# Optimization experiments

Measured on AMD Instinct MI355X. Metric: run time of the kernel, lower is better.

## Reference

```python
import jax, jax.numpy as jnp
import numpy as np

WIN = 7           # window height/width
DIM = 192         # channels
HEADS = 6
HEAD_DIM = DIM // HEADS  # 32
B_WIN = 4096      # num_windows * batch
NW = 64           # windows per image (for shift mask)
N = WIN * WIN     # 49 tokens per window
THETA = 10.0


def _init_rope_freqs(key):
    # init_random_2d_freqs: mag = 1/theta^(arange(0,hd,4)[:hd//4]/hd)
    mag = 1.0 / THETA ** (jnp.arange(0, HEAD_DIM, 4)[: HEAD_DIM // 4].astype(jnp.float32) / HEAD_DIM)
    ang = jax.random.uniform(key, (HEADS, 1)) * 2.0 * jnp.pi
    fx = jnp.concatenate([mag * jnp.cos(ang), mag * jnp.cos(jnp.pi / 2 + ang)], axis=-1)  # [H, hd/2]
    fy = jnp.concatenate([mag * jnp.sin(ang), mag * jnp.sin(jnp.pi / 2 + ang)], axis=-1)
    return jnp.stack([fx, fy], axis=0)  # [2, H, hd/2]


def setup_inputs() -> dict:
    key = jax.random.key(0)
    ks = jax.random.split(key, 6)
    x = jax.random.normal(ks[0], (B_WIN, N, DIM), dtype=jnp.float32)
    mask = jnp.zeros((NW, N, N), dtype=jnp.float32)  # 0/-inf shift mask (zeros: no shift)
    qkv_w = jax.random.normal(ks[1], (3 * DIM, DIM), dtype=jnp.float32) * 0.02
    qkv_b = jnp.zeros((3 * DIM,), dtype=jnp.float32)
    proj_w = jax.random.normal(ks[2], (DIM, DIM), dtype=jnp.float32) * 0.02
    proj_b = jnp.zeros((DIM,), dtype=jnp.float32)
    rope_freqs = _init_rope_freqs(ks[3])
    return {"x": x, "mask": mask, "qkv_w": qkv_w, "qkv_b": qkv_b,
            "proj_w": proj_w, "proj_b": proj_b, "rope_freqs": rope_freqs}


def _rope_angles(rope_freqs):
    # t_x = t % end_x, t_y = t // end_x over the flattened window grid
    t = jnp.arange(N, dtype=jnp.float32)
    t_x = jnp.mod(t, WIN)
    t_y = jnp.floor_divide(t, WIN)
    # angle[h, n, d] = t_x[n]*fx[h,d] + t_y[n]*fy[h,d]  -> [H, N, hd/2]
    ang = (t_x[None, :, None] * rope_freqs[0][:, None, :]
           + t_y[None, :, None] * rope_freqs[1][:, None, :])
    return jnp.cos(ang), jnp.sin(ang)


def _apply_rope(u, cos, sin):
    # u: [B, H, N, hd]; complex multiply on (even, odd) pairs
    b, h, n, d = u.shape
    ur = u.reshape(b, h, n, d // 2, 2)
    re = ur[..., 0] * cos - ur[..., 1] * sin
    im = ur[..., 0] * sin + ur[..., 1] * cos
    return jnp.stack([re, im], axis=-1).reshape(b, h, n, d)


def reference(x, mask, qkv_w, qkv_b, proj_w, proj_b, rope_freqs):
    B_, n, C = x.shape
    H, hd = HEADS, HEAD_DIM
    scale = hd ** -0.5
    qkv = (x @ qkv_w.T + qkv_b).reshape(B_, n, 3, H, hd)
    qkv = jnp.transpose(qkv, (2, 0, 3, 1, 4))          # [3, B, H, N, hd]
    q, k, v = qkv[0] * scale, qkv[1], qkv[2]
    cos, sin = _rope_angles(rope_freqs)                 # [H, N, hd/2]
    q = _apply_rope(q, cos, sin)
    k = _apply_rope(k, cos, sin)
    attn = jnp.einsum('bhnd,bhmd->bhnm', q, k)          # [B, H, N, N]
    nW = mask.shape[0]
    attn = attn.reshape(B_ // nW, nW, H, n, n) + mask[None, :, None]
    attn = jax.nn.softmax(attn.reshape(B_, H, n, n), axis=-1)
    out = jnp.einsum('bhnm,bhmd->bhnd', attn, v)        # [B, H, N, hd]
    out = jnp.transpose(out, (0, 2, 1, 3)).reshape(B_, n, C)
    return out @ proj_w.T + proj_b
```

## Files before the change

kernel.cpp:

```cpp
#include <hip/hip_runtime.h>

#define NTOK 49
#define DIM 192
#define HEADS 6
#define NWIN 64
#define NBLK 4096

typedef unsigned short u16;
typedef short bf16x8 __attribute__((ext_vector_type(8)));
typedef unsigned short u16x4 __attribute__((ext_vector_type(4)));
typedef unsigned short u16x8 __attribute__((ext_vector_type(8)));
typedef float f32x4 __attribute__((ext_vector_type(4)));

#define Q_OFF    0
#define K_OFF    20000
#define PS_OFF   40000
#define VT_OFF   49216
#define XS_OFF   49216
#define OS_OFF   20000
#define MK_OFF   76864
#define LDS_TOTAL 81764

#define QKVW_ELEMS (3 * DIM * DIM)
#define PROJW_ELEMS (DIM * DIM)

__device__ __forceinline__ float bf2f(u16 u) {
    union { unsigned int i; float f; } x; x.i = ((unsigned int)u) << 16; return x.f;
}
__device__ __forceinline__ u16 f2bf(float f) {
    union { float f; unsigned int u; } x; x.f = f;
    unsigned int u = x.u;
    u += 0x7fffu + ((u >> 16) & 1u);
    return (u16)(u >> 16);
}

extern "C" __global__ void __launch_bounds__(256)
convert_weights(const float* __restrict__ qkv_w, const float* __restrict__ proj_w,
                u16* __restrict__ ws) {
    int i = (blockIdx.x * 256 + threadIdx.x) * 4;
    if (i >= QKVW_ELEMS + PROJW_ELEMS) return;
    const float* s = (i < QKVW_ELEMS) ? (qkv_w + i) : (proj_w + (i - QKVW_ELEMS));
    float4 v = *(const float4*)s;
    ushort4 o;
    o.x = f2bf(v.x); o.y = f2bf(v.y); o.z = f2bf(v.z); o.w = f2bf(v.w);
    *(ushort4*)(ws + i) = o;
}

extern "C" __global__ void __launch_bounds__(256, 2)
fused_win_attn(const float* __restrict__ x, const float* __restrict__ mask,
               const u16* __restrict__ wsq, const float* __restrict__ qkv_b,
               const u16* __restrict__ wsp, const float* __restrict__ proj_b,
               const float* __restrict__ rfreq, float* __restrict__ out)
{
    extern __shared__ __align__(16) char smem[];
    u16* qsm = (u16*)(smem + Q_OFF);
    u16* ksm = (u16*)(smem + K_OFF);
    u16* ps  = (u16*)(smem + PS_OFF);
    u16* vt  = (u16*)(smem + VT_OFF);
    u16* xs  = (u16*)(smem + XS_OFF);
    float* os = (float*)(smem + OS_OFF);
    u16* ao  = (u16*)(smem + Q_OFF);
    u16* mk  = (u16*)(smem + MK_OFF);

    const int tid  = threadIdx.x;
    const int wave = tid >> 6;
    const int lane = tid & 63;
    const int ln   = lane & 15;
    const int quad = lane >> 4;
    const int blk  = blockIdx.x;
    const int widx = blk & (NWIN - 1);
    const float* xg = x + (long)blk * NTOK * DIM;

    const f32x4 fzero = {0.f, 0.f, 0.f, 0.f};

    for (int i = tid; i < NTOK * 48; i += 256) {
        int r = i / 48, c = (i % 48) * 4;
        float4 v = *(const float4*)(xg + r * DIM + c);
        u16x4 o = { f2bf(v.x), f2bf(v.y), f2bf(v.z), f2bf(v.w) };
        *(u16x4*)(xs + r * 200 + c) = o;
    }
    {
        u16x8 zz = {0,0,0,0,0,0,0,0};
        for (int i = tid; i < 15 * 25; i += 256) {
            int r = 49 + i / 25, c = (i % 25) * 8;
            *(u16x8*)(xs + r * 200 + c) = zz;
        }
        if (tid < 50) {
            int c = (tid % 25) * 8;
            u16* base = (tid < 25) ? qsm : ksm;
            *(u16x8*)(base + 49 * 200 + c) = zz;
        }
    }
    for (int i = tid; i < NTOK * NTOK; i += 256) {
        int n = i / NTOK, m = i % NTOK;
        mk[n * 50 + m] = f2bf(mask[widx * (NTOK * NTOK) + i]);
    }
    __syncthreads();

    bf16x8 bfrag[6][4];
    #pragma unroll
    for (int kk = 0; kk < 6; kk++)
        #pragma unroll
        for (int nt = 0; nt < 4; nt++)
            bfrag[kk][nt] = *(const bf16x8*)(xs + (nt * 16 + ln) * 200 + kk * 32 + quad * 8);
    __syncthreads();

    const float scale = 0.17677669529663687f;
    for (int jt = wave; jt < 36; jt += 4) {
        bf16x8 af[6];
        const u16* wr = wsq + (jt * 16 + ln) * DIM + quad * 8;
        #pragma unroll
        for (int kk = 0; kk < 6; kk++) af[kk] = *(const bf16x8*)(wr + kk * 32);
        f32x4 acc[4];
        #pragma unroll
        for (int nt = 0; nt < 4; nt++) acc[nt] = fzero;
        #pragma unroll
        for (int kk = 0; kk < 6; kk++)
            #pragma unroll
            for (int nt = 0; nt < 4; nt++)
                acc[nt] = __builtin_amdgcn_mfma_f32_16x16x32_bf16(af[kk], bfrag[kk][nt], acc[nt], 0, 0, 0);

        int j0 = jt * 16 + quad * 4;
        int qkvi = j0 / DIM;
        int c0 = j0 % DIM;
        int h  = c0 >> 5;
        int p0 = (c0 & 31) >> 1;
        float b0 = qkv_b[j0],   b1 = qkv_b[j0+1];
        float b2 = qkv_b[j0+2], b3 = qkv_b[j0+3];
        float fx0 = rfreq[h*16+p0],   fy0 = rfreq[96+h*16+p0];
        float fx1 = rfreq[h*16+p0+1], fy1 = rfreq[96+h*16+p0+1];
        #pragma unroll
        for (int nt = 0; nt < 4; nt++) {
            int t = nt * 16 + ln;
            float v0 = acc[nt][0] + b0;
            float v1 = acc[nt][1] + b1;
            float v2 = acc[nt][2] + b2;
            float v3 = acc[nt][3] + b3;
            if (qkvi < 2) {
                float tx = (float)(t % 7), ty = (float)(t / 7);
                float a0 = tx * fx0 + ty * fy0;
                float a1 = tx * fx1 + ty * fy1;
                float s0, c0s, s1, c1s;
                __sincosf(a0, &s0, &c0s);
                __sincosf(a1, &s1, &c1s);
                float r0 = v0 * c0s - v1 * s0;
                float i0 = v0 * s0  + v1 * c0s;
                float r1 = v2 * c1s - v3 * s1;
                float i1 = v2 * s1  + v3 * c1s;
                if (qkvi == 0) { r0 *= scale; i0 *= scale; r1 *= scale; i1 *= scale; }
                if (t < NTOK) {
                    u16x4 pk = { f2bf(r0), f2bf(i0), f2bf(r1), f2bf(i1) };
                    u16* dst = (qkvi == 0 ? qsm : ksm) + t * 200 + c0;
                    *(u16x4*)dst = pk;
                }
            } else {
                float w0 = (t < NTOK) ? v0 : 0.f;
                float w1 = (t < NTOK) ? v1 : 0.f;
                float w2 = (t < NTOK) ? v2 : 0.f;
                float w3 = (t < NTOK) ? v3 : 0.f;
                vt[(c0+0)*72 + t] = f2bf(w0);
                vt[(c0+1)*72 + t] = f2bf(w1);
                vt[(c0+2)*72 + t] = f2bf(w2);
                vt[(c0+3)*72 + t] = f2bf(w3);
            }
        }
    }
    __syncthreads();

    int qrow = wave * 16 + ln; if (qrow > NTOK) qrow = NTOK;
    for (int h = 0; h < HEADS; h++) {
        f32x4 s4[4];
        bf16x8 aq = *(const bf16x8*)(qsm + qrow * 200 + h * 32 + quad * 8);
        #pragma unroll
        for (int nt = 0; nt < 4; nt++) {
            int krow = nt * 16 + ln; if (krow > NTOK) krow = NTOK;
            bf16x8 bk = *(const bf16x8*)(ksm + krow * 200 + h * 32 + quad * 8);
            s4[nt] = __builtin_amdgcn_mfma_f32_16x16x32_bf16(aq, bk, fzero, 0, 0, 0);
        }
        #pragma unroll
        for (int nt = 0; nt < 4; nt++) {
            int m = nt * 16 + ln;
            #pragma unroll
            for (int r = 0; r < 4; r++) {
                int n = wave * 16 + quad * 4 + r;
                if (m >= NTOK) s4[nt][r] = -1e30f;
                else if (n < NTOK) s4[nt][r] += bf2f(mk[n * 50 + m]);
            }
        }
        float mx[4], sm[4], rs[4];
        #pragma unroll
        for (int r = 0; r < 4; r++) {
            float v = fmaxf(fmaxf(s4[0][r], s4[1][r]), fmaxf(s4[2][r], s4[3][r]));
            #pragma unroll
            for (int d = 1; d < 16; d <<= 1) v = fmaxf(v, __shfl_xor(v, d));
            mx[r] = v; sm[r] = 0.f;
        }
        #pragma unroll
        for (int nt = 0; nt < 4; nt++) {
            int m = nt * 16 + ln;
            #pragma unroll
            for (int r = 0; r < 4; r++) {
                float e = __expf(s4[nt][r] - mx[r]);
                sm[r] += e;
                ps[(wave * 16 + quad * 4 + r) * 72 + m] = f2bf(e);
            }
        }
        #pragma unroll
        for (int r = 0; r < 4; r++) {
            float v = sm[r];
            #pragma unroll
            for (int d = 1; d < 16; d <<= 1) v += __shfl_xor(v, d);
            rs[r] = 1.0f / v;
        }
        f32x4 o0 = fzero, o1 = fzero;
        #pragma unroll
        for (int kk = 0; kk < 2; kk++) {
            bf16x8 ap  = *(const bf16x8*)(ps + (wave * 16 + ln) * 72 + kk * 32 + quad * 8);
            bf16x8 bv0 = *(const bf16x8*)(vt + (h * 32 + ln) * 72      + kk * 32 + quad * 8);
            bf16x8 bv1 = *(const bf16x8*)(vt + (h * 32 + 16 + ln) * 72 + kk * 32 + quad * 8);
            o0 = __builtin_amdgcn_mfma_f32_16x16x32_bf16(ap, bv0, o0, 0, 0, 0);
            o1 = __builtin_amdgcn_mfma_f32_16x16x32_bf16(ap, bv1, o1, 0, 0, 0);
        }
        #pragma unroll
        for (int r = 0; r < 4; r++) {
            int t = wave * 16 + quad * 4 + r;
            if (t < NTOK) {
                ao[t * 200 + h * 32 + ln]      = f2bf(o0[r] * rs[r]);
                ao[t * 200 + h * 32 + 16 + ln] = f2bf(o1[r] * rs[r]);
            }
        }
    }
    __syncthreads();

    bf16x8 aa[6];
    int arow = wave * 16 + ln; if (arow > NTOK) arow = NTOK;
    #pragma unroll
    for (int kk = 0; kk < 6; kk++)
        aa[kk] = *(const bf16x8*)(ao + arow * 200 + kk * 32 + quad * 8);
    for (int nt = 0; nt < 12; nt++) {
        const u16* wp = wsp + (nt * 16 + ln) * DIM + quad * 8;
        f32x4 p4 = fzero;
        #pragma unroll
        for (int kk = 0; kk < 6; kk++) {
            bf16x8 bw = *(const bf16x8*)(wp + kk * 32);
            p4 = __builtin_amdgcn_mfma_f32_16x16x32_bf16(aa[kk], bw, p4, 0, 0, 0);
        }
        float bb = proj_b[nt * 16 + ln];
        #pragma unroll
        for (int r = 0; r < 4; r++) {
            int t = wave * 16 + quad * 4 + r;
            os[t * 196 + nt * 16 + ln] = p4[r] + bb;
        }
    }
    __syncthreads();

    float* og = out + (long)blk * NTOK * DIM;
    for (int i = tid; i < NTOK * 48; i += 256) {
        int r = i / 48, c = (i % 48) * 4;
        *(float4*)(og + r * DIM + c) = *(const float4*)(os + r * 196 + c);
    }
}

extern "C" void kernel_launch(void* const* d_in, const int* in_sizes, int n_in,
                              void* d_out, int out_size, void* d_ws, size_t ws_size,
                              hipStream_t stream) {
    (void)in_sizes; (void)n_in; (void)out_size; (void)ws_size;
    u16* ws = (u16*)d_ws;
    convert_weights<<<dim3((QKVW_ELEMS + PROJW_ELEMS) / 4 / 256 + 1), dim3(256), 0, stream>>>(
        (const float*)d_in[2], (const float*)d_in[4], ws);
    hipFuncSetAttribute(reinterpret_cast<const void*>(fused_win_attn),
                        hipFuncAttributeMaxDynamicSharedMemorySize, LDS_TOTAL);
    fused_win_attn<<<dim3(NBLK), dim3(256), LDS_TOTAL, stream>>>(
        (const float*)d_in[0], (const float*)d_in[1],
        ws, (const float*)d_in[3],
        ws + QKVW_ELEMS, (const float*)d_in[5],
        (const float*)d_in[6], (float*)d_out);
}
```

Before: 618.2 us.

## Split fused window attention into QKV+RoPE and attention+projection kernels

```diff
diff --git a/kernel.cpp b/kernel.cpp
--- a/kernel.cpp
+++ b/kernel.cpp
@@ -11,6 +11,16 @@
 typedef unsigned short u16x4 __attribute__((ext_vector_type(4)));
 typedef unsigned short u16x8 __attribute__((ext_vector_type(8)));
 typedef float f32x4 __attribute__((ext_vector_type(4)));
+
+#define QKVW_ELEMS (3 * DIM * DIM)
+#define PROJW_ELEMS (DIM * DIM)
+
+#define TB_OFF_BYTES ((QKVW_ELEMS + PROJW_ELEMS) * 2)
+#define TB_QUADS     (HEADS * NTOK * 8)
+#define QG_OFF_U16   ((TB_OFF_BYTES + TB_QUADS * 16) / 2)
+#define QG_ELEMS     (NBLK * NTOK * DIM)
+#define KG_OFF_U16   (QG_OFF_U16 + QG_ELEMS)
+#define WS_NEEDED_BYTES (((size_t)KG_OFF_U16 + (size_t)QG_ELEMS) * 2)
 
 #define Q_OFF    0
 #define K_OFF    20000
@@ -20,9 +30,6 @@
 #define OS_OFF   20000
 #define MK_OFF   76864
 #define LDS_TOTAL 81764
-
-#define QKVW_ELEMS (3 * DIM * DIM)
-#define PROJW_ELEMS (DIM * DIM)
 
 __device__ __forceinline__ float bf2f(u16 u) {
     union { unsigned int i; float f; } x; x.i = ((unsigned int)u) << 16; return x.f;
@@ -44,6 +51,253 @@
     ushort4 o;
     o.x = f2bf(v.x); o.y = f2bf(v.y); o.z = f2bf(v.z); o.w = f2bf(v.w);
     *(ushort4*)(ws + i) = o;
+}
+
+extern "C" __global__ void __launch_bounds__(256)
+rope_table(const float* __restrict__ rfreq, float* __restrict__ tb) {
+    int i = blockIdx.x * 256 + threadIdx.x;
+    if (i >= TB_QUADS) return;
+    int h = i / (NTOK * 8);
+    int r = i % (NTOK * 8);
+    int t = r >> 3;
+    int p0 = (r & 7) * 2;
+    float tx = (float)(t % 7), ty = (float)(t / 7);
+    float a0 = tx * rfreq[h * 16 + p0]     + ty * rfreq[96 + h * 16 + p0];
+    float a1 = tx * rfreq[h * 16 + p0 + 1] + ty * rfreq[96 + h * 16 + p0 + 1];
+    float4 o;
+    o.x = cosf(a0); o.y = sinf(a0);
+    o.z = cosf(a1); o.w = sinf(a1);
+    ((float4*)tb)[i] = o;
+}
+
+extern "C" __global__ void __launch_bounds__(256, 3)
+qkv_rope(const float* __restrict__ x, const u16* __restrict__ wsq,
+         const float* __restrict__ qkv_b, const float* __restrict__ tb,
+         u16* __restrict__ qg, u16* __restrict__ kg, u16* __restrict__ vg)
+{
+    __shared__ __align__(16) char smem[40000];
+    u16* qs = (u16*)(smem);
+    u16* ks = (u16*)(smem + 20000);
+    u16* xs = (u16*)(smem + 14400);
+
+    const int tid  = threadIdx.x;
+    const int wave = tid >> 6;
+    const int lane = tid & 63;
+    const int ln   = lane & 15;
+    const int quad = lane >> 4;
+    const int blk  = blockIdx.x;
+    const float* xg = x + (long)blk * NTOK * DIM;
+    const f32x4 fzero = {0.f, 0.f, 0.f, 0.f};
+
+    for (int i = tid; i < NTOK * 48; i += 256) {
+        int r = i / 48, c = (i % 48) * 4;
+        float4 v = *(const float4*)(xg + r * DIM + c);
+        u16x4 o = { f2bf(v.x), f2bf(v.y), f2bf(v.z), f2bf(v.w) };
+        *(u16x4*)(xs + r * 200 + c) = o;
+    }
+    {
+        u16x8 zz = {0,0,0,0,0,0,0,0};
+        for (int i = tid; i < 15 * 25; i += 256) {
+            int r = 49 + i / 25, c = (i % 25) * 8;
+            *(u16x8*)(xs + r * 200 + c) = zz;
+        }
+    }
+    __syncthreads();
+
+    bf16x8 bfrag[6][4];
+    #pragma unroll
+    for (int kk = 0; kk < 6; kk++)
+        #pragma unroll
+        for (int nt = 0; nt < 4; nt++)
+            bfrag[kk][nt] = *(const bf16x8*)(xs + (nt * 16 + ln) * 200 + kk * 32 + quad * 8);
+    __syncthreads();
+
+    const float scale = 0.17677669529663687f;
+    u16* vb = vg + (long)blk * (NTOK * DIM * 2);
+
+    for (int jt = wave; jt < 36; jt += 4) {
+        bf16x8 af[6];
+        const u16* wr = wsq + (jt * 16 + ln) * DIM + quad * 8;
+        #pragma unroll
+        for (int kk = 0; kk < 6; kk++) af[kk] = *(const bf16x8*)(wr + kk * 32);
+        f32x4 acc[4];
+        #pragma unroll
+        for (int nt = 0; nt < 4; nt++) acc[nt] = fzero;
+        #pragma unroll
+        for (int kk = 0; kk < 6; kk++)
+            #pragma unroll
+            for (int nt = 0; nt < 4; nt++)
+                acc[nt] = __builtin_amdgcn_mfma_f32_16x16x32_bf16(af[kk], bfrag[kk][nt], acc[nt], 0, 0, 0);
+
+        int j0 = jt * 16 + quad * 4;
+        int qkvi = j0 / DIM;
+        int c0 = j0 % DIM;
+        int h  = c0 >> 5;
+        int p0 = (c0 & 31) >> 1;
+        float b0 = qkv_b[j0],   b1 = qkv_b[j0+1];
+        float b2 = qkv_b[j0+2], b3 = qkv_b[j0+3];
+        #pragma unroll
+        for (int nt = 0; nt < 4; nt++) {
+            int t = nt * 16 + ln;
+            float v0 = acc[nt][0] + b0;
+            float v1 = acc[nt][1] + b1;
+            float v2 = acc[nt][2] + b2;
+            float v3 = acc[nt][3] + b3;
+            if (qkvi < 2) {
+                if (t < NTOK) {
+                    float4 tv = ((const float4*)tb)[(h * NTOK + t) * 8 + (p0 >> 1)];
+                    float r0 = v0 * tv.x - v1 * tv.y;
+                    float i0 = v0 * tv.y + v1 * tv.x;
+                    float r1 = v2 * tv.z - v3 * tv.w;
+                    float i1 = v2 * tv.w + v3 * tv.z;
+                    if (qkvi == 0) { r0 *= scale; i0 *= scale; r1 *= scale; i1 *= scale; }
+                    u16x4 pk = { f2bf(r0), f2bf(i0), f2bf(r1), f2bf(i1) };
+                    *(u16x4*)((qkvi == 0 ? qs : ks) + t * 200 + c0) = pk;
+                }
+            } else {
+                float w0 = (t < NTOK) ? v0 : 0.f;
+                float w1 = (t < NTOK) ? v1 : 0.f;
+                float w2 = (t < NTOK) ? v2 : 0.f;
+                float w3 = (t < NTOK) ? v3 : 0.f;
+                vb[(c0+0)*64 + t] = f2bf(w0);
+                vb[(c0+1)*64 + t] = f2bf(w1);
+                vb[(c0+2)*64 + t] = f2bf(w2);
+                vb[(c0+3)*64 + t] = f2bf(w3);
+            }
+        }
+    }
+    __syncthreads();
+
+    u16* qgb = qg + (long)blk * (NTOK * DIM);
+    u16* kgb = kg + (long)blk * (NTOK * DIM);
+    for (int i = tid; i < 2 * NTOK * 24; i += 256) {
+        int isk = i >= NTOK * 24;
+        int j = isk ? i - NTOK * 24 : i;
+        int r = j / 24, c = (j % 24) * 8;
+        u16x8 vv = *(const u16x8*)((isk ? ks : qs) + r * 200 + c);
+        *(u16x8*)((isk ? kgb : qgb) + r * DIM + c) = vv;
+    }
+}
+
+extern "C" __global__ void __launch_bounds__(256, 4)
+attn_proj(const float* __restrict__ mask, const u16* __restrict__ qg,
+          const u16* __restrict__ kg, const u16* __restrict__ wsp,
+          const float* __restrict__ proj_b, float* __restrict__ out)
+{
+    __shared__ __align__(16) char smem[34128];
+    u16* ao = (u16*)(smem);
+    u16* ps = (u16*)(smem + 20000);
+    u16* mk = (u16*)(smem + 29216);
+
+    const int tid  = threadIdx.x;
+    const int wave = tid >> 6;
+    const int lane = tid & 63;
+    const int ln   = lane & 15;
+    const int quad = lane >> 4;
+    const int blk  = blockIdx.x;
+    const int widx = blk & (NWIN - 1);
+    const f32x4 fzero = {0.f, 0.f, 0.f, 0.f};
+
+    for (int i = tid; i < NTOK * NTOK; i += 256) {
+        int n = i / NTOK, m = i % NTOK;
+        mk[n * 50 + m] = f2bf(mask[widx * (NTOK * NTOK) + i]);
+    }
+    if (tid < 25) {
+        u16x8 zz = {0,0,0,0,0,0,0,0};
+        *(u16x8*)(ao + 49 * 200 + tid * 8) = zz;
+    }
+    __syncthreads();
+
+    const u16* qb = qg + (long)blk * (NTOK * DIM);
+    const u16* kb = kg + (long)blk * (NTOK * DIM);
+    const u16* vb = (const u16*)out + (long)blk * (NTOK * DIM * 2);
+
+    int qrow = wave * 16 + ln; if (qrow > 48) qrow = 48;
+    for (int h = 0; h < HEADS; h++) {
+        f32x4 s4[4];
+        bf16x8 aq = *(const bf16x8*)(qb + qrow * DIM + h * 32 + quad * 8);
+        #pragma unroll
+        for (int nt = 0; nt < 4; nt++) {
+            int krow = nt * 16 + ln; if (krow > 48) krow = 48;
+            bf16x8 bk = *(const bf16x8*)(kb + krow * DIM + h * 32 + quad * 8);
+            s4[nt] = __builtin_amdgcn_mfma_f32_16x16x32_bf16(aq, bk, fzero, 0, 0, 0);
+        }
+        #pragma unroll
+        for (int nt = 0; nt < 4; nt++) {
+            int m = nt * 16 + ln;
+            #pragma unroll
+            for (int r = 0; r < 4; r++) {
+                int n = wave * 16 + quad * 4 + r;
+                if (m >= NTOK) s4[nt][r] = -1e30f;
+                else if (n < NTOK) s4[nt][r] += bf2f(mk[n * 50 + m]);
+            }
+        }
+        float mx[4], sm[4], rs[4];
+        #pragma unroll
+        for (int r = 0; r < 4; r++) {
+            float v = fmaxf(fmaxf(s4[0][r], s4[1][r]), fmaxf(s4[2][r], s4[3][r]));
+            #pragma unroll
+            for (int d = 1; d < 16; d <<= 1) v = fmaxf(v, __shfl_xor(v, d));
+            mx[r] = v; sm[r] = 0.f;
+        }
+        #pragma unroll
+        for (int nt = 0; nt < 4; nt++) {
+            int m = nt * 16 + ln;
+            #pragma unroll
+            for (int r = 0; r < 4; r++) {
+                float e = __expf(s4[nt][r] - mx[r]);
+                sm[r] += e;
+                ps[(wave * 16 + quad * 4 + r) * 72 + m] = f2bf(e);
+            }
+        }
+        #pragma unroll
+        for (int r = 0; r < 4; r++) {
+            float v = sm[r];
+            #pragma unroll
+            for (int d = 1; d < 16; d <<= 1) v += __shfl_xor(v, d);
+            rs[r] = 1.0f / v;
+        }
+        f32x4 o0 = fzero, o1 = fzero;
+        #pragma unroll
+        for (int kk = 0; kk < 2; kk++) {
+            bf16x8 ap  = *(const bf16x8*)(ps + (wave * 16 + ln) * 72 + kk * 32 + quad * 8);
+            bf16x8 bv0 = *(const bf16x8*)(vb + (h * 32 + ln) * 64      + kk * 32 + quad * 8);
+            bf16x8 bv1 = *(const bf16x8*)(vb + (h * 32 + 16 + ln) * 64 + kk * 32 + quad * 8);
+            o0 = __builtin_amdgcn_mfma_f32_16x16x32_bf16(ap, bv0, o0, 0, 0, 0);
+            o1 = __builtin_amdgcn_mfma_f32_16x16x32_bf16(ap, bv1, o1, 0, 0, 0);
+        }
+        #pragma unroll
+        for (int r = 0; r < 4; r++) {
+            int t = wave * 16 + quad * 4 + r;
+            if (t < NTOK) {
+                ao[t * 200 + h * 32 + ln]      = f2bf(o0[r] * rs[r]);
+                ao[t * 200 + h * 32 + 16 + ln] = f2bf(o1[r] * rs[r]);
+            }
+        }
+    }
+    __syncthreads();
+
+    bf16x8 aa[6];
+    int arow = wave * 16 + ln; if (arow > NTOK) arow = NTOK;
+    #pragma unroll
+    for (int kk = 0; kk < 6; kk++)
+        aa[kk] = *(const bf16x8*)(ao + arow * 200 + kk * 32 + quad * 8);
+    float* ob = out + (long)blk * (NTOK * DIM);
+    for (int nt = 0; nt < 12; nt++) {
+        const u16* wp = wsp + (nt * 16 + ln) * DIM + quad * 8;
+        f32x4 p4 = fzero;
+        #pragma unroll
+        for (int kk = 0; kk < 6; kk++) {
+            bf16x8 bw = *(const bf16x8*)(wp + kk * 32);
+            p4 = __builtin_amdgcn_mfma_f32_16x16x32_bf16(aa[kk], bw, p4, 0, 0, 0);
+        }
+        float bb = proj_b[nt * 16 + ln];
+        #pragma unroll
+        for (int r = 0; r < 4; r++) {
+            int t = wave * 16 + quad * 4 + r;
+            if (t < NTOK) ob[t * DIM + nt * 16 + ln] = p4[r] + bb;
+        }
+    }
 }
 
 extern "C" __global__ void __launch_bounds__(256, 2)
@@ -264,15 +518,28 @@
 extern "C" void kernel_launch(void* const* d_in, const int* in_sizes, int n_in,
                               void* d_out, int out_size, void* d_ws, size_t ws_size,
                               hipStream_t stream) {
-    (void)in_sizes; (void)n_in; (void)out_size; (void)ws_size;
+    (void)in_sizes; (void)n_in; (void)out_size;
     u16* ws = (u16*)d_ws;
     convert_weights<<<dim3((QKVW_ELEMS + PROJW_ELEMS) / 4 / 256 + 1), dim3(256), 0, stream>>>(
         (const float*)d_in[2], (const float*)d_in[4], ws);
-    hipFuncSetAttribute(reinterpret_cast<const void*>(fused_win_attn),
-                        hipFuncAttributeMaxDynamicSharedMemorySize, LDS_TOTAL);
-    fused_win_attn<<<dim3(NBLK), dim3(256), LDS_TOTAL, stream>>>(
-        (const float*)d_in[0], (const float*)d_in[1],
-        ws, (const float*)d_in[3],
-        ws + QKVW_ELEMS, (const float*)d_in[5],
-        (const float*)d_in[6], (float*)d_out);
-}
+    if (ws_size >= WS_NEEDED_BYTES) {
+        float* tb = (float*)((char*)d_ws + TB_OFF_BYTES);
+        rope_table<<<dim3((TB_QUADS + 255) / 256), dim3(256), 0, stream>>>(
+            (const float*)d_in[6], tb);
+        u16* qg = ws + QG_OFF_U16;
+        u16* kg = ws + KG_OFF_U16;
+        qkv_rope<<<dim3(NBLK), dim3(256), 0, stream>>>(
+            (const float*)d_in[0], ws, (const float*)d_in[3], tb, qg, kg, (u16*)d_out);
+        attn_proj<<<dim3(NBLK), dim3(256), 0, stream>>>(
+            (const float*)d_in[1], qg, kg, ws + QKVW_ELEMS, (const float*)d_in[5],
+            (float*)d_out);
+    } else {
+        hipFuncSetAttribute(reinterpret_cast<const void*>(fused_win_attn),
+                            hipFuncAttributeMaxDynamicSharedMemorySize, LDS_TOTAL);
+        fused_win_attn<<<dim3(NBLK), dim3(256), LDS_TOTAL, stream>>>(
+            (const float*)d_in[0], (const float*)d_in[1],
+            ws, (const float*)d_in[3],
+            ws + QKVW_ELEMS, (const float*)d_in[5],
+            (const float*)d_in[6], (float*)d_out);
+    }
+}
```

Measured after the change: 683.7 us. +10.6%, slower.

## Shrink LDS footprint: keep Q/mask in registers, stage V in global scratch, precompute RoPE

Applied to the files above, without the earlier changes.

```diff
diff --git a/kernel.cpp b/kernel.cpp
--- a/kernel.cpp
+++ b/kernel.cpp
@@ -12,17 +12,18 @@
 typedef unsigned short u16x8 __attribute__((ext_vector_type(8)));
 typedef float f32x4 __attribute__((ext_vector_type(4)));
 
-#define Q_OFF    0
-#define K_OFF    20000
-#define PS_OFF   40000
-#define VT_OFF   49216
-#define XS_OFF   49216
-#define OS_OFF   20000
-#define MK_OFF   76864
-#define LDS_TOTAL 81764
-
 #define QKVW_ELEMS (3 * DIM * DIM)
 #define PROJW_ELEMS (DIM * DIM)
+
+#define TB_OFF_BYTES ((QKVW_ELEMS + PROJW_ELEMS) * 2)
+#define TB_QUADS     (HEADS * NTOK * 8)
+
+#define XS_OFF 0
+#define AO_OFF 0
+#define BN_OFF 25600
+#define KS_OFF 25600
+#define PS_OFF 45200
+#define LDS_TOTAL 52256
 
 __device__ __forceinline__ float bf2f(u16 u) {
     union { unsigned int i; float f; } x; x.i = ((unsigned int)u) << 16; return x.f;
@@ -46,21 +47,35 @@
     *(ushort4*)(ws + i) = o;
 }
 
-extern "C" __global__ void __launch_bounds__(256, 2)
+extern "C" __global__ void __launch_bounds__(256)
+rope_table(const float* __restrict__ rfreq, float* __restrict__ tb) {
+    int i = blockIdx.x * 256 + threadIdx.x;
+    if (i >= TB_QUADS) return;
+    int h = i / (NTOK * 8);
+    int r = i % (NTOK * 8);
+    int t = r >> 3;
+    int p0 = (r & 7) * 2;
+    float tx = (float)(t % 7), ty = (float)(t / 7);
+    float a0 = tx * rfreq[h * 16 + p0]     + ty * rfreq[96 + h * 16 + p0];
+    float a1 = tx * rfreq[h * 16 + p0 + 1] + ty * rfreq[96 + h * 16 + p0 + 1];
+    float4 o;
+    o.x = cosf(a0); o.y = sinf(a0);
+    o.z = cosf(a1); o.w = sinf(a1);
+    ((float4*)tb)[i] = o;
+}
+
+extern "C" __global__ void __launch_bounds__(256, 3)
 fused_win_attn(const float* __restrict__ x, const float* __restrict__ mask,
                const u16* __restrict__ wsq, const float* __restrict__ qkv_b,
                const u16* __restrict__ wsp, const float* __restrict__ proj_b,
-               const float* __restrict__ rfreq, float* __restrict__ out)
+               const float* __restrict__ tb, float* __restrict__ out)
 {
-    extern __shared__ __align__(16) char smem[];
-    u16* qsm = (u16*)(smem + Q_OFF);
-    u16* ksm = (u16*)(smem + K_OFF);
-    u16* ps  = (u16*)(smem + PS_OFF);
-    u16* vt  = (u16*)(smem + VT_OFF);
-    u16* xs  = (u16*)(smem + XS_OFF);
-    float* os = (float*)(smem + OS_OFF);
-    u16* ao  = (u16*)(smem + Q_OFF);
-    u16* mk  = (u16*)(smem + MK_OFF);
+    __shared__ __align__(16) char smem[LDS_TOTAL];
+    u16* xs = (u16*)(smem + XS_OFF);
+    u16* ao = (u16*)(smem + AO_OFF);
+    u16* bn = (u16*)(smem + BN_OFF);
+    u16* ks = (u16*)(smem + KS_OFF);
+    u16* ps = (u16*)(smem + PS_OFF);
 
     const int tid  = threadIdx.x;
     const int wave = tid >> 6;
@@ -70,8 +85,23 @@
     const int blk  = blockIdx.x;
     const int widx = blk & (NWIN - 1);
     const float* xg = x + (long)blk * NTOK * DIM;
-
     const f32x4 fzero = {0.f, 0.f, 0.f, 0.f};
+    const float2* tb2 = (const float2*)tb;
+    const float scale = 0.17677669529663687f;
+
+    u16* vb = (u16*)out + (long)blk * (NTOK * DIM * 2);
+
+    float mreg[4][4];
+    #pragma unroll
+    for (int nt = 0; nt < 4; nt++) {
+        int m = nt * 16 + ln;
+        #pragma unroll
+        for (int r = 0; r < 4; r++) {
+            int n = wave * 16 + quad * 4 + r;
+            mreg[nt][r] = (m >= NTOK) ? -1e30f
+                         : ((n < NTOK) ? mask[widx * (NTOK * NTOK) + n * NTOK + m] : 0.f);
+        }
+    }
 
     for (int i = tid; i < NTOK * 48; i += 256) {
         int r = i / 48, c = (i % 48) * 4;
@@ -85,50 +115,69 @@
             int r = 49 + i / 25, c = (i % 25) * 8;
             *(u16x8*)(xs + r * 200 + c) = zz;
         }
-        if (tid < 50) {
-            int c = (tid % 25) * 8;
-            u16* base = (tid < 25) ? qsm : ksm;
-            *(u16x8*)(base + 49 * 200 + c) = zz;
-        }
-    }
-    for (int i = tid; i < NTOK * NTOK; i += 256) {
-        int n = i / NTOK, m = i % NTOK;
-        mk[n * 50 + m] = f2bf(mask[widx * (NTOK * NTOK) + i]);
     }
     __syncthreads();
 
-    bf16x8 bfrag[6][4];
+    bf16x8 bfragA[6];
     #pragma unroll
     for (int kk = 0; kk < 6; kk++)
-        #pragma unroll
-        for (int nt = 0; nt < 4; nt++)
-            bfrag[kk][nt] = *(const bf16x8*)(xs + (nt * 16 + ln) * 200 + kk * 32 + quad * 8);
-    __syncthreads();
-
-    const float scale = 0.17677669529663687f;
-    for (int jt = wave; jt < 36; jt += 4) {
+        bfragA[kk] = *(const bf16x8*)(xs + (wave * 16 + ln) * 200 + kk * 32 + quad * 8);
+
+    for (int jt = 0; jt < 12; jt++) {
         bf16x8 af[6];
         const u16* wr = wsq + (jt * 16 + ln) * DIM + quad * 8;
         #pragma unroll
         for (int kk = 0; kk < 6; kk++) af[kk] = *(const bf16x8*)(wr + kk * 32);
+        f32x4 acc = fzero;
+        #pragma unroll
+        for (int kk = 0; kk < 6; kk++)
+            acc = __builtin_amdgcn_mfma_f32_16x16x32_bf16(bfragA[kk], af[kk], acc, 0, 0, 0);
+
+        int ch = jt * 16 + ln;
+        int hh = jt >> 1;
+        int p  = ((jt & 1) << 3) + (ln >> 1);
+        float b = qkv_b[ch];
+        float ssgn = (ln & 1) ? 1.f : -1.f;
+        #pragma unroll
+        for (int r = 0; r < 4; r++) {
+            int t = wave * 16 + quad * 4 + r;
+            float v = acc[r] + b;
+            float prt = __shfl_xor(v, 1);
+            int tl = (t < NTOK) ? t : NTOK - 1;
+            float2 cs = tb2[(hh * NTOK + tl) * 16 + p];
+            float o = v * cs.x + prt * (ssgn * cs.y);
+            if (t < NTOK) bn[t * 200 + ch] = f2bf(o * scale);
+        }
+    }
+    bf16x8 qreg[6];
+    #pragma unroll
+    for (int h = 0; h < 6; h++)
+        qreg[h] = *(const bf16x8*)(bn + (wave * 16 + ln) * 200 + h * 32 + quad * 8);
+    __syncthreads();
+
+    for (int jt = 12 + wave; jt < 36; jt += 4) {
+        bf16x8 af[6];
+        const u16* wr = wsq + (jt * 16 + ln) * DIM + quad * 8;
+        #pragma unroll
+        for (int kk = 0; kk < 6; kk++) af[kk] = *(const bf16x8*)(wr + kk * 32);
         f32x4 acc[4];
         #pragma unroll
         for (int nt = 0; nt < 4; nt++) acc[nt] = fzero;
         #pragma unroll
         for (int kk = 0; kk < 6; kk++)
             #pragma unroll
-            for (int nt = 0; nt < 4; nt++)
-                acc[nt] = __builtin_amdgcn_mfma_f32_16x16x32_bf16(af[kk], bfrag[kk][nt], acc[nt], 0, 0, 0);
+            for (int nt = 0; nt < 4; nt++) {
+                bf16x8 bx = *(const bf16x8*)(xs + (nt * 16 + ln) * 200 + kk * 32 + quad * 8);
+                acc[nt] = __builtin_amdgcn_mfma_f32_16x16x32_bf16(af[kk], bx, acc[nt], 0, 0, 0);
+            }
 
         int j0 = jt * 16 + quad * 4;
-        int qkvi = j0 / DIM;
+        int isv = (jt >= 24);
         int c0 = j0 % DIM;
-        int h  = c0 >> 5;
+        int hh = c0 >> 5;
         int p0 = (c0 & 31) >> 1;
         float b0 = qkv_b[j0],   b1 = qkv_b[j0+1];
         float b2 = qkv_b[j0+2], b3 = qkv_b[j0+3];
-        float fx0 = rfreq[h*16+p0],   fy0 = rfreq[96+h*16+p0];
-        float fx1 = rfreq[h*16+p0+1], fy1 = rfreq[96+h*16+p0+1];
         #pragma unroll
         for (int nt = 0; nt < 4; nt++) {
             int t = nt * 16 + ln;
@@ -136,57 +185,44 @@
             float v1 = acc[nt][1] + b1;
             float v2 = acc[nt][2] + b2;
             float v3 = acc[nt][3] + b3;
-            if (qkvi < 2) {
-                float tx = (float)(t % 7), ty = (float)(t / 7);
-                float a0 = tx * fx0 + ty * fy0;
-                float a1 = tx * fx1 + ty * fy1;
-                float s0, c0s, s1, c1s;
-                __sincosf(a0, &s0, &c0s);
-                __sincosf(a1, &s1, &c1s);
-                float r0 = v0 * c0s - v1 * s0;
-                float i0 = v0 * s0  + v1 * c0s;
-                float r1 = v2 * c1s - v3 * s1;
-                float i1 = v2 * s1  + v3 * c1s;
-                if (qkvi == 0) { r0 *= scale; i0 *= scale; r1 *= scale; i1 *= scale; }
+            if (!isv) {
                 if (t < NTOK) {
+                    float4 tv = ((const float4*)tb)[(hh * NTOK + t) * 8 + (p0 >> 1)];
+                    float r0 = v0 * tv.x - v1 * tv.y;
+                    float i0 = v0 * tv.y + v1 * tv.x;
+                    float r1 = v2 * tv.z - v3 * tv.w;
+                    float i1 = v2 * tv.w + v3 * tv.z;
                     u16x4 pk = { f2bf(r0), f2bf(i0), f2bf(r1), f2bf(i1) };
-                    u16* dst = (qkvi == 0 ? qsm : ksm) + t * 200 + c0;
-                    *(u16x4*)dst = pk;
+                    *(u16x4*)(ks + t * 200 + c0) = pk;
                 }
             } else {
                 float w0 = (t < NTOK) ? v0 : 0.f;
                 float w1 = (t < NTOK) ? v1 : 0.f;
                 float w2 = (t < NTOK) ? v2 : 0.f;
                 float w3 = (t < NTOK) ? v3 : 0.f;
-                vt[(c0+0)*72 + t] = f2bf(w0);
-                vt[(c0+1)*72 + t] = f2bf(w1);
-                vt[(c0+2)*72 + t] = f2bf(w2);
-                vt[(c0+3)*72 + t] = f2bf(w3);
+                vb[(c0+0)*64 + t] = f2bf(w0);
+                vb[(c0+1)*64 + t] = f2bf(w1);
+                vb[(c0+2)*64 + t] = f2bf(w2);
+                vb[(c0+3)*64 + t] = f2bf(w3);
             }
         }
     }
     __syncthreads();
 
-    int qrow = wave * 16 + ln; if (qrow > NTOK) qrow = NTOK;
+    #pragma unroll
     for (int h = 0; h < HEADS; h++) {
         f32x4 s4[4];
-        bf16x8 aq = *(const bf16x8*)(qsm + qrow * 200 + h * 32 + quad * 8);
         #pragma unroll
         for (int nt = 0; nt < 4; nt++) {
-            int krow = nt * 16 + ln; if (krow > NTOK) krow = NTOK;
-            bf16x8 bk = *(const bf16x8*)(ksm + krow * 200 + h * 32 + quad * 8);
-            s4[nt] = __builtin_amdgcn_mfma_f32_16x16x32_bf16(aq, bk, fzero, 0, 0, 0);
-        }
-        #pragma unroll
-        for (int nt = 0; nt < 4; nt++) {
-            int m = nt * 16 + ln;
-            #pragma unroll
-            for (int r = 0; r < 4; r++) {
-                int n = wave * 16 + quad * 4 + r;
-                if (m >= NTOK) s4[nt][r] = -1e30f;
-                else if (n < NTOK) s4[nt][r] += bf2f(mk[n * 50 + m]);
-            }
-        }
+            int krow = nt * 16 + ln; if (krow > NTOK - 1) krow = NTOK - 1;
+            bf16x8 bk = *(const bf16x8*)(ks + krow * 200 + h * 32 + quad * 8);
+            s4[nt] = __builtin_amdgcn_mfma_f32_16x16x32_bf16(qreg[h], bk, fzero, 0, 0, 0);
+        }
+        #pragma unroll
+        for (int nt = 0; nt < 4; nt++)
+            #pragma unroll
+            for (int r = 0; r < 4; r++)
+                s4[nt][r] += mreg[nt][r];
         float mx[4], sm[4], rs[4];
         #pragma unroll
         for (int r = 0; r < 4; r++) {
@@ -202,7 +238,8 @@
             for (int r = 0; r < 4; r++) {
                 float e = __expf(s4[nt][r] - mx[r]);
                 sm[r] += e;
-                ps[(wave * 16 + quad * 4 + r) * 72 + m] = f2bf(e);
+                int prow = wave * 16 + quad * 4 + r;
+                if (prow < NTOK) ps[prow * 72 + m] = f2bf(e);
             }
         }
         #pragma unroll
@@ -215,9 +252,10 @@
         f32x4 o0 = fzero, o1 = fzero;
         #pragma unroll
         for (int kk = 0; kk < 2; kk++) {
-            bf16x8 ap  = *(const bf16x8*)(ps + (wave * 16 + ln) * 72 + kk * 32 + quad * 8);
-            bf16x8 bv0 = *(const bf16x8*)(vt + (h * 32 + ln) * 72      + kk * 32 + quad * 8);
-            bf16x8 bv1 = *(const bf16x8*)(vt + (h * 32 + 16 + ln) * 72 + kk * 32 + quad * 8);
+            int arow = wave * 16 + ln; if (arow > NTOK - 1) arow = NTOK - 1;
+            bf16x8 ap  = *(const bf16x8*)(ps + arow * 72 + kk * 32 + quad * 8);
+            bf16x8 bv0 = *(const bf16x8*)(vb + (h * 32 + ln) * 64      + kk * 32 + quad * 8);
+            bf16x8 bv1 = *(const bf16x8*)(vb + (h * 32 + 16 + ln) * 64 + kk * 32 + quad * 8);
             o0 = __builtin_amdgcn_mfma_f32_16x16x32_bf16(ap, bv0, o0, 0, 0, 0);
             o1 = __builtin_amdgcn_mfma_f32_16x16x32_bf16(ap, bv1, o1, 0, 0, 0);
         }
@@ -233,10 +271,11 @@
     __syncthreads();
 
     bf16x8 aa[6];
-    int arow = wave * 16 + ln; if (arow > NTOK) arow = NTOK;
+    int arow = wave * 16 + ln; if (arow > NTOK - 1) arow = NTOK - 1;
     #pragma unroll
     for (int kk = 0; kk < 6; kk++)
         aa[kk] = *(const bf16x8*)(ao + arow * 200 + kk * 32 + quad * 8);
+    float* ob = out + (long)blk * (NTOK * DIM);
     for (int nt = 0; nt < 12; nt++) {
         const u16* wp = wsp + (nt * 16 + ln) * DIM + quad * 8;
         f32x4 p4 = fzero;
@@ -249,15 +288,8 @@
         #pragma unroll
         for (int r = 0; r < 4; r++) {
             int t = wave * 16 + quad * 4 + r;
-            os[t * 196 + nt * 16 + ln] = p4[r] + bb;
-        }
-    }
-    __syncthreads();
-
-    float* og = out + (long)blk * NTOK * DIM;
-    for (int i = tid; i < NTOK * 48; i += 256) {
-        int r = i / 48, c = (i % 48) * 4;
-        *(float4*)(og + r * DIM + c) = *(const float4*)(os + r * 196 + c);
+            if (t < NTOK) ob[t * DIM + nt * 16 + ln] = p4[r] + bb;
+        }
     }
 }
 
@@ -268,11 +300,12 @@
     u16* ws = (u16*)d_ws;
     convert_weights<<<dim3((QKVW_ELEMS + PROJW_ELEMS) / 4 / 256 + 1), dim3(256), 0, stream>>>(
         (const float*)d_in[2], (const float*)d_in[4], ws);
-    hipFuncSetAttribute(reinterpret_cast<const void*>(fused_win_attn),
-                        hipFuncAttributeMaxDynamicSharedMemorySize, LDS_TOTAL);
-    fused_win_attn<<<dim3(NBLK), dim3(256), LDS_TOTAL, stream>>>(
+    float* tb = (float*)((char*)d_ws + TB_OFF_BYTES);
+    rope_table<<<dim3((TB_QUADS + 255) / 256), dim3(256), 0, stream>>>(
+        (const float*)d_in[6], tb);
+    fused_win_attn<<<dim3(NBLK), dim3(256), 0, stream>>>(
         (const float*)d_in[0], (const float*)d_in[1],
         ws, (const float*)d_in[3],
         ws + QKVW_ELEMS, (const float*)d_in[5],
-        (const float*)d_in[6], (float*)d_out);
-}
+        tb, (float*)d_out);
+}
```

New measurement: 741.0 us. 1.2x slower.
